# Performance work log

Measured on AMD Instinct MI355X. Metric: run time of the kernel, lower is better.

Reference implementation:

```python
import jax, jax.numpy as jnp
import numpy as np

H = 16  # num heads
ROPE_BASE = 10000.0

def _rope(t):
    # t: [B, T, H, D]; half-split (rotate_half / LLaMA-style) rotary embedding
    B, T, nH, D = t.shape
    half = D // 2
    inv_freq = 1.0 / (ROPE_BASE ** (jnp.arange(0, half, dtype=jnp.float32) / half))
    ang = jnp.arange(T, dtype=jnp.float32)[:, None] * inv_freq[None, :]  # [T, half]
    cos = jnp.cos(ang)[None, :, None, :]  # [1,T,1,half]
    sin = jnp.sin(ang)[None, :, None, :]
    t1, t2 = t[..., :half], t[..., half:]
    return jnp.concatenate([t1 * cos - t2 * sin, t2 * cos + t1 * sin], axis=-1)

def setup_inputs() -> dict:
    key = jax.random.key(0)
    ks = jax.random.split(key, 5)
    B, T, C = 2, 2048, 1024
    s = 1.0 / np.sqrt(C)
    return {
        "x": jax.random.normal(ks[0], (B, T, C), jnp.float32),
        "Wqkv": jax.random.normal(ks[1], (C, 3 * C), jnp.float32) * s,
        "bqkv": jnp.zeros((3 * C,), jnp.float32),
        "Wout": jax.random.normal(ks[2], (C, C), jnp.float32) * s,
        "bout": jnp.zeros((C,), jnp.float32),
    }

def reference(x, Wqkv, bqkv, Wout, bout):
    B, T, C = x.shape
    D = C // H
    qkv = (x @ Wqkv + bqkv).reshape(B, T, 3, H, D)
    q, k, v = qkv[:, :, 0], qkv[:, :, 1], qkv[:, :, 2]  # [B,T,H,D]
    q = _rope(q)
    k = _rope(k)
    scale = 1.0 / jnp.sqrt(jnp.asarray(D, x.dtype))
    scores = jnp.einsum('bqhd,bkhd->bhqk', q, k) * scale
    probs = jax.nn.softmax(scores, axis=-1)
    attn = jnp.einsum('bhqk,bkhd->bqhd', probs, v).reshape(B, T, C)
    return attn @ Wout + bout
```

## Files before the change

### kernel.cpp

```cpp
#include <hip/hip_runtime.h>

typedef float f32x4 __attribute__((ext_vector_type(4)));
typedef short bf16x8 __attribute__((ext_vector_type(8)));
typedef short bf16x4 __attribute__((ext_vector_type(4)));

#define DEV __device__ __forceinline__

DEV unsigned short f2bf(float x) {
  union { float f; unsigned u; } v; v.f = x;
  unsigned r = v.u + 0x7fffu + ((v.u >> 16) & 1u);
  return (unsigned short)(r >> 16);
}
DEV float bf2f(unsigned short h) {
  union { unsigned u; float f; } v; v.u = ((unsigned)h) << 16;
  return v.f;
}

#if defined(__has_builtin)
# if __has_builtin(__builtin_amdgcn_global_load_lds)
#  define HAVE_GLL 1
# endif
# if __has_builtin(__builtin_amdgcn_exp2f)
#  define EXP2(x) __builtin_amdgcn_exp2f(x)
# else
#  define EXP2(x) exp2f(x)
# endif
#else
# define EXP2(x) exp2f(x)
#endif

DEV unsigned pk_bf16_trunc(float a, float b) {
  return __builtin_amdgcn_perm(__float_as_uint(b), __float_as_uint(a), 0x07060302u);
}
DEV unsigned pk_bf16_rnd(float a, float b) {
  return ((unsigned)f2bf(b) << 16) | f2bf(a);
}

DEV void g2l16(const unsigned short* g, unsigned short* l) {
#ifdef HAVE_GLL
  __builtin_amdgcn_global_load_lds((const __attribute__((address_space(1))) void*)g,
                                   (__attribute__((address_space(3))) void*)l, 16, 0, 0);
#else
  *(uint4*)l = *(const uint4*)g;
#endif
}

DEV f32x4 mfma16x16x16(bf16x4 a, bf16x4 b, f32x4 c) {
#if defined(__has_builtin) && __has_builtin(__builtin_amdgcn_mfma_f32_16x16x16bf16_1k)
  return __builtin_amdgcn_mfma_f32_16x16x16bf16_1k(a, b, c, 0, 0, 0);
#else
  asm volatile("v_mfma_f32_16x16x16_bf16 %0, %1, %2, %0" : "+v"(c) : "v"(a), "v"(b));
  return c;
#endif
}

__global__ void rope_tab(float* cosb, float* sinb) {
  int i = blockIdx.x * 256 + threadIdx.x;
  int t = i >> 5, d = i & 31;
  float invf = (float)(1.0 / pow(10000.0, (double)d / 32.0));
  float ang = (float)t * invf;
  cosb[i] = (float)cos((double)ang);
  sinb[i] = (float)sin((double)ang);
}

__global__ void castA(const float* __restrict__ in, unsigned short* __restrict__ out) {
  int i = blockIdx.x * 256 + threadIdx.x;
  f32x4 v = ((const f32x4*)in)[i];
  ushort4 o;
  o.x = f2bf(v[0]); o.y = f2bf(v[1]); o.z = f2bf(v[2]); o.w = f2bf(v[3]);
  ((ushort4*)out)[i] = o;
}

__global__ __launch_bounds__(256) void transW(const float* __restrict__ W,
                                              unsigned short* __restrict__ Wt, int N) {
  __shared__ float t[64 * 65];
  int k0 = blockIdx.x * 64, n0 = blockIdx.y * 64;
  for (int idx = threadIdx.x; idx < 4096; idx += 256) {
    int kl = idx >> 6, nl = idx & 63;
    t[kl * 65 + nl] = W[(size_t)(k0 + kl) * N + n0 + nl];
  }
  __syncthreads();
  for (int idx = threadIdx.x; idx < 4096; idx += 256) {
    int nl = idx >> 6, kl = idx & 63;
    Wt[(size_t)(n0 + nl) * 1024 + k0 + kl] = f2bf(t[kl * 65 + nl]);
  }
}

#define QSCALE 0.180336880f
__global__ __launch_bounds__(256, 2) void gemm_qkv(
    const unsigned short* __restrict__ A, const unsigned short* __restrict__ Bt,
    const float* __restrict__ bias, const float* __restrict__ cosb,
    const float* __restrict__ sinb, unsigned short* __restrict__ QK,
    unsigned short* __restrict__ Vt) {
  const int K = 1024;
  __shared__ alignas(16) unsigned short As[128 * 64];
  __shared__ alignas(16) unsigned short Bs[128 * 64];
  const int tid = threadIdx.x;
  const int lane = tid & 63, wave = tid >> 6;
  const int l15 = lane & 15, quad = lane >> 4;
  const int m0 = blockIdx.y * 128, n0 = blockIdx.x * 128;
  const int wm = (wave & 1) * 64, wn = (wave >> 1) * 64;

  f32x4 acc[4][4];
#pragma unroll
  for (int i = 0; i < 4; i++)
#pragma unroll
    for (int j = 0; j < 4; j++)
#pragma unroll
      for (int r = 0; r < 4; r++) acc[i][j][r] = 0.f;

  for (int kt = 0; kt < 16; ++kt) {
    __syncthreads();
#pragma unroll
    for (int i = 0; i < 4; ++i) {
      int u = i * 256 + tid;
      int row = u >> 3;
      int kcg = (u & 7) ^ (row & 7);
      g2l16(A  + (size_t)(m0 + row) * K + (kt << 6) + (kcg << 3), As + u * 8);
      g2l16(Bt + (size_t)(n0 + row) * K + (kt << 6) + (kcg << 3), Bs + u * 8);
    }
    __syncthreads();
#pragma unroll
    for (int ks = 0; ks < 2; ++ks) {
      const int kc = ks * 4 + quad;
      bf16x8 af[4], bfr[4];
#pragma unroll
      for (int t = 0; t < 4; ++t) {
        int mrow = wm + t * 16 + l15;
        af[t] = *(const bf16x8*)(As + (mrow * 8 + (kc ^ (mrow & 7))) * 8);
        int nrow = wn + t * 16 + l15;
        bfr[t] = *(const bf16x8*)(Bs + (nrow * 8 + (kc ^ (nrow & 7))) * 8);
      }
#pragma unroll
      for (int mt = 0; mt < 4; ++mt)
#pragma unroll
        for (int nt = 0; nt < 4; ++nt)
          acc[mt][nt] = __builtin_amdgcn_mfma_f32_16x16x32_bf16(af[mt], bfr[nt], acc[mt][nt], 0, 0, 0);
    }
  }
  const int headcol = n0 + wn;
  const int b = m0 >> 11;
  float bb[4];
#pragma unroll
  for (int nt = 0; nt < 4; ++nt) bb[nt] = bias[headcol + nt * 16 + l15];

  if (headcol < 2048) {
    const float scale = (headcol < 1024) ? QSCALE : 1.f;
#pragma unroll
    for (int mt = 0; mt < 4; ++mt) {
#pragma unroll
      for (int r = 0; r < 4; ++r) {
        int row = m0 + wm + mt * 16 + quad * 4 + r;
        int t = row & 2047;
#pragma unroll
        for (int nt = 0; nt < 2; ++nt) {
          int d = nt * 16 + l15;
          float c = cosb[t * 32 + d], s = sinb[t * 32 + d];
          float v1 = acc[mt][nt][r] + bb[nt];
          float v2 = acc[mt][nt + 2][r] + bb[nt + 2];
          QK[(size_t)row * 2048 + headcol + d]      = f2bf((v1 * c - v2 * s) * scale);
          QK[(size_t)row * 2048 + headcol + d + 32] = f2bf((v2 * c + v1 * s) * scale);
        }
      }
    }
  } else {
    const int hv = (headcol - 2048) >> 6;
    const int t0 = (m0 + wm) & 2047;
#pragma unroll
    for (int mt = 0; mt < 4; ++mt)
#pragma unroll
      for (int nt = 0; nt < 4; ++nt) {
        int d = nt * 16 + l15;
        uint2 w;
        w.x = pk_bf16_rnd(acc[mt][nt][0] + bb[nt], acc[mt][nt][1] + bb[nt]);
        w.y = pk_bf16_rnd(acc[mt][nt][2] + bb[nt], acc[mt][nt][3] + bb[nt]);
        *(uint2*)(Vt + ((size_t)((b * 16 + hv) * 64 + d)) * 2048 + t0 + mt * 16 + quad * 4) = w;
      }
  }
}

__global__ __launch_bounds__(256, 2) void gemm64(
    const unsigned short* __restrict__ A, const unsigned short* __restrict__ Bt,
    const float* __restrict__ bias, float* __restrict__ C, int M, int N, int K) {
  __shared__ alignas(16) unsigned short As[64 * 64];
  __shared__ alignas(16) unsigned short Bs[128 * 64];
  const int tid = threadIdx.x;
  const int lane = tid & 63, wave = tid >> 6;
  const int l15 = lane & 15, quad = lane >> 4;
  const int m0 = blockIdx.y * 64, n0 = blockIdx.x * 128;
  const int wm = (wave & 1) * 32, wn = (wave >> 1) * 64;

  f32x4 acc[2][4];
#pragma unroll
  for (int i = 0; i < 2; i++)
#pragma unroll
    for (int j = 0; j < 4; j++)
#pragma unroll
      for (int r = 0; r < 4; r++) acc[i][j][r] = 0.f;

  const int nkt = K >> 6;
  for (int kt = 0; kt < nkt; ++kt) {
    __syncthreads();
#pragma unroll
    for (int i = 0; i < 2; ++i) {
      int u = i * 256 + tid;
      int row = u >> 3;
      int kcg = (u & 7) ^ (row & 7);
      g2l16(A + (size_t)(m0 + row) * K + (kt << 6) + (kcg << 3), As + u * 8);
    }
#pragma unroll
    for (int i = 0; i < 4; ++i) {
      int u = i * 256 + tid;
      int row = u >> 3;
      int kcg = (u & 7) ^ (row & 7);
      g2l16(Bt + (size_t)(n0 + row) * K + (kt << 6) + (kcg << 3), Bs + u * 8);
    }
    __syncthreads();
#pragma unroll
    for (int ks = 0; ks < 2; ++ks) {
      const int kc = ks * 4 + quad;
      bf16x8 af[2], bfr[4];
#pragma unroll
      for (int t = 0; t < 2; ++t) {
        int mrow = wm + t * 16 + l15;
        af[t] = *(const bf16x8*)(As + (mrow * 8 + (kc ^ (mrow & 7))) * 8);
      }
#pragma unroll
      for (int t = 0; t < 4; ++t) {
        int nrow = wn + t * 16 + l15;
        bfr[t] = *(const bf16x8*)(Bs + (nrow * 8 + (kc ^ (nrow & 7))) * 8);
      }
#pragma unroll
      for (int mt = 0; mt < 2; ++mt)
#pragma unroll
        for (int nt = 0; nt < 4; ++nt)
          acc[mt][nt] = __builtin_amdgcn_mfma_f32_16x16x32_bf16(af[mt], bfr[nt], acc[mt][nt], 0, 0, 0);
    }
  }
#pragma unroll
  for (int mt = 0; mt < 2; ++mt)
#pragma unroll
    for (int nt = 0; nt < 4; ++nt) {
      int col = n0 + wn + nt * 16 + l15;
      int rowb = m0 + wm + mt * 16 + quad * 4;
      float b = bias[col];
#pragma unroll
      for (int r = 0; r < 4; ++r)
        C[(size_t)(rowb + r) * N + col] = acc[mt][nt][r] + b;
    }
}

__global__ __launch_bounds__(128, 2) void flash_attn(const unsigned short* __restrict__ QK,
                                                     const unsigned short* __restrict__ Vt,
                                                     unsigned short* __restrict__ O) {
  __shared__ alignas(16) unsigned short Ks[64 * 64];
  __shared__ alignas(16) unsigned short Vs[64 * 64];
  const int tid = threadIdx.x, lane = tid & 63, wave = tid >> 6;
  const int l15 = lane & 15, quad = lane >> 4;
  const int bh = blockIdx.x, qb = blockIdx.y;
  const int b = bh >> 4, h = bh & 15;
  const int q0 = qb * 64 + wave * 32;
  bf16x8 qf[2][2];
#pragma unroll
  for (int ks = 0; ks < 2; ++ks)
#pragma unroll
    for (int qg = 0; qg < 2; ++qg)
      qf[ks][qg] = *(const bf16x8*)(QK + (size_t)(b * 2048 + q0 + qg * 16 + l15) * 2048 +
                                    h * 64 + ks * 32 + quad * 8);
  f32x4 o[2][4];
#pragma unroll
  for (int qg = 0; qg < 2; qg++)
#pragma unroll
    for (int nt = 0; nt < 4; nt++)
#pragma unroll
      for (int r = 0; r < 4; r++) o[qg][nt][r] = 0.f;
  float li[2] = {0.f, 0.f};
  const f32x4 negb = {-12.f, -12.f, -12.f, -12.f};

  for (int kb = 0; kb < 32; ++kb) {
    __syncthreads();
#pragma unroll
    for (int i = 0; i < 4; ++i) {
      int u = i * 128 + tid;
      int row = u >> 3;
      int cg = (u & 7) ^ (row & 7);
      g2l16(QK + (size_t)(b * 2048 + kb * 64 + row) * 2048 + 1024 + h * 64 + cg * 8, Ks + u * 8);
      g2l16(Vt + ((size_t)bh * 64 + row) * 2048 + kb * 64 + cg * 8, Vs + u * 8);
    }
    __syncthreads();
    f32x4 sacc[2][4];
#pragma unroll
    for (int ks = 0; ks < 2; ++ks) {
      const int kc = ks * 4 + quad;
#pragma unroll
      for (int mt = 0; mt < 4; ++mt) {
        int key = mt * 16 + l15;
        bf16x8 kf = *(const bf16x8*)(Ks + (key * 8 + (kc ^ (key & 7))) * 8);
        if (ks == 0) {
          sacc[0][mt] = __builtin_amdgcn_mfma_f32_16x16x32_bf16(kf, qf[0][0], negb, 0, 0, 0);
          sacc[1][mt] = __builtin_amdgcn_mfma_f32_16x16x32_bf16(kf, qf[0][1], negb, 0, 0, 0);
        } else {
          sacc[0][mt] = __builtin_amdgcn_mfma_f32_16x16x32_bf16(kf, qf[1][0], sacc[0][mt], 0, 0, 0);
          sacc[1][mt] = __builtin_amdgcn_mfma_f32_16x16x32_bf16(kf, qf[1][1], sacc[1][mt], 0, 0, 0);
        }
      }
    }
    bf16x4 vf[4][4];
#pragma unroll
    for (int nt = 0; nt < 4; ++nt)
#pragma unroll
      for (int mt = 0; mt < 4; ++mt) {
        int dd = nt * 16 + l15;
        int cg = mt * 2 + (quad >> 1);
        vf[nt][mt] = *(const bf16x4*)(Vs + (dd * 8 + (cg ^ (dd & 7))) * 8 + (quad & 1) * 4);
      }
#pragma unroll
    for (int qg = 0; qg < 2; ++qg) {
      bf16x4 pf[4];
      float psum = 0.f;
#pragma unroll
      for (int mt = 0; mt < 4; ++mt) {
        float p0 = EXP2(sacc[qg][mt][0]);
        float p1 = EXP2(sacc[qg][mt][1]);
        float p2 = EXP2(sacc[qg][mt][2]);
        float p3 = EXP2(sacc[qg][mt][3]);
        psum += (p0 + p1) + (p2 + p3);
        union { uint2 u; bf16x4 v; } cc;
        cc.u.x = pk_bf16_trunc(p0, p1);
        cc.u.y = pk_bf16_trunc(p2, p3);
        pf[mt] = cc.v;
      }
      li[qg] += psum;
#pragma unroll
      for (int nt = 0; nt < 4; ++nt)
#pragma unroll
        for (int mt = 0; mt < 4; ++mt)
          o[qg][nt] = mfma16x16x16(vf[nt][mt], pf[mt], o[qg][nt]);
    }
  }
#pragma unroll
  for (int qg = 0; qg < 2; ++qg) {
    li[qg] += __shfl_xor(li[qg], 16);
    li[qg] += __shfl_xor(li[qg], 32);
    float inv = 1.001953125f / li[qg];
    size_t rowb = (size_t)(b * 2048 + q0 + qg * 16 + l15) * 1024 + h * 64;
#pragma unroll
    for (int nt = 0; nt < 4; ++nt) {
      uint2 w;
      w.x = pk_bf16_rnd(o[qg][nt][0] * inv, o[qg][nt][1] * inv);
      w.y = pk_bf16_rnd(o[qg][nt][2] * inv, o[qg][nt][3] * inv);
      *(uint2*)(O + rowb + nt * 16 + quad * 4) = w;
    }
  }
}

extern "C" void kernel_launch(void* const* d_in, const int* in_sizes, int n_in,
                              void* d_out, int out_size, void* d_ws, size_t ws_size,
                              hipStream_t stream) {
  const float* x    = (const float*)d_in[0];
  const float* Wqkv = (const float*)d_in[1];
  const float* bqkv = (const float*)d_in[2];
  const float* Wout = (const float*)d_in[3];
  const float* bout = (const float*)d_in[4];
  float* out = (float*)d_out;
  char* ws = (char*)d_ws;
  float*          COS  = (float*)(ws + 0);
  float*          SIN  = (float*)(ws + 262144);
  unsigned short* A1   = (unsigned short*)(ws + 524288);
  unsigned short* W1t  = (unsigned short*)(ws + 8912896);
  unsigned short* W2t  = (unsigned short*)(ws + 15204352);
  unsigned short* QK   = (unsigned short*)(ws + 17301504);
  unsigned short* VT   = (unsigned short*)(ws + 34078720);
  unsigned short* A2   = (unsigned short*)(ws + 42467328);

  rope_tab<<<256, 256, 0, stream>>>(COS, SIN);
  castA<<<4096, 256, 0, stream>>>(x, A1);
  transW<<<dim3(16, 48), 256, 0, stream>>>(Wqkv, W1t, 3072);
  transW<<<dim3(16, 16), 256, 0, stream>>>(Wout, W2t, 1024);
  gemm_qkv<<<dim3(24, 32), 256, 0, stream>>>(A1, W1t, bqkv, COS, SIN, QK, VT);
  flash_attn<<<dim3(32, 32), 128, 0, stream>>>(QK, VT, A2);
  gemm64<<<dim3(8, 64), 256, 0, stream>>>(A2, W2t, bout, out, 4096, 1024, 1024);
}
```

Measured before the change: 191.5 us.

## Fuse prep kernels into one launch and enlarge flash-attention tiles to 128x128

After: 181.5 us. 5.2% less time.

```diff
diff --git a/kernel.cpp b/kernel.cpp
--- a/kernel.cpp
+++ b/kernel.cpp
@@ -54,27 +54,36 @@
 #endif
 }
 
-__global__ void rope_tab(float* cosb, float* sinb) {
-  int i = blockIdx.x * 256 + threadIdx.x;
-  int t = i >> 5, d = i & 31;
-  float invf = (float)(1.0 / pow(10000.0, (double)d / 32.0));
-  float ang = (float)t * invf;
-  cosb[i] = (float)cos((double)ang);
-  sinb[i] = (float)sin((double)ang);
-}
-
-__global__ void castA(const float* __restrict__ in, unsigned short* __restrict__ out) {
-  int i = blockIdx.x * 256 + threadIdx.x;
-  f32x4 v = ((const f32x4*)in)[i];
-  ushort4 o;
-  o.x = f2bf(v[0]); o.y = f2bf(v[1]); o.z = f2bf(v[2]); o.w = f2bf(v[3]);
-  ((ushort4*)out)[i] = o;
-}
-
-__global__ __launch_bounds__(256) void transW(const float* __restrict__ W,
-                                              unsigned short* __restrict__ Wt, int N) {
+__global__ __launch_bounds__(256) void prep(const float* __restrict__ x,
+                                            const float* __restrict__ Wqkv,
+                                            const float* __restrict__ Wout,
+                                            float* cosb, float* sinb,
+                                            unsigned short* __restrict__ A1,
+                                            unsigned short* __restrict__ W1t,
+                                            unsigned short* __restrict__ W2t) {
   __shared__ float t[64 * 65];
-  int k0 = blockIdx.x * 64, n0 = blockIdx.y * 64;
+  int blk = blockIdx.x;
+  if (blk < 256) {
+    int i = blk * 256 + threadIdx.x;
+    int tt = i >> 5, d = i & 31;
+    float invf = (float)(1.0 / pow(10000.0, (double)d / 32.0));
+    float ang = (float)tt * invf;
+    cosb[i] = (float)cos((double)ang);
+    sinb[i] = (float)sin((double)ang);
+    return;
+  }
+  if (blk < 4352) {
+    int i = (blk - 256) * 256 + threadIdx.x;
+    f32x4 v = ((const f32x4*)x)[i];
+    ushort4 o;
+    o.x = f2bf(v[0]); o.y = f2bf(v[1]); o.z = f2bf(v[2]); o.w = f2bf(v[3]);
+    ((ushort4*)A1)[i] = o;
+    return;
+  }
+  const float* W; unsigned short* Wt; int N, bidx;
+  if (blk < 5120) { W = Wqkv; Wt = W1t; N = 3072; bidx = blk - 4352; }
+  else            { W = Wout; Wt = W2t; N = 1024; bidx = blk - 5120; }
+  int k0 = (bidx & 15) * 64, n0 = (bidx >> 4) * 64;
   for (int idx = threadIdx.x; idx < 4096; idx += 256) {
     int kl = idx >> 6, nl = idx & 63;
     t[kl * 65 + nl] = W[(size_t)(k0 + kl) * N + n0 + nl];
@@ -250,16 +259,16 @@
     }
 }
 
-__global__ __launch_bounds__(128, 2) void flash_attn(const unsigned short* __restrict__ QK,
+__global__ __launch_bounds__(256, 2) void flash_attn(const unsigned short* __restrict__ QK,
                                                      const unsigned short* __restrict__ Vt,
                                                      unsigned short* __restrict__ O) {
-  __shared__ alignas(16) unsigned short Ks[64 * 64];
-  __shared__ alignas(16) unsigned short Vs[64 * 64];
+  __shared__ alignas(16) unsigned short Ks[128 * 64];
+  __shared__ alignas(16) unsigned short Vs[64 * 128];
   const int tid = threadIdx.x, lane = tid & 63, wave = tid >> 6;
   const int l15 = lane & 15, quad = lane >> 4;
   const int bh = blockIdx.x, qb = blockIdx.y;
   const int b = bh >> 4, h = bh & 15;
-  const int q0 = qb * 64 + wave * 32;
+  const int q0 = qb * 128 + wave * 32;
   bf16x8 qf[2][2];
 #pragma unroll
   for (int ks = 0; ks < 2; ++ks)
@@ -277,23 +286,26 @@
   float li[2] = {0.f, 0.f};
   const f32x4 negb = {-12.f, -12.f, -12.f, -12.f};
 
-  for (int kb = 0; kb < 32; ++kb) {
+  for (int kb = 0; kb < 16; ++kb) {
     __syncthreads();
 #pragma unroll
     for (int i = 0; i < 4; ++i) {
-      int u = i * 128 + tid;
-      int row = u >> 3;
-      int cg = (u & 7) ^ (row & 7);
-      g2l16(QK + (size_t)(b * 2048 + kb * 64 + row) * 2048 + 1024 + h * 64 + cg * 8, Ks + u * 8);
-      g2l16(Vt + ((size_t)bh * 64 + row) * 2048 + kb * 64 + cg * 8, Vs + u * 8);
-    }
-    __syncthreads();
-    f32x4 sacc[2][4];
+      int u = i * 256 + tid;
+      int krow = u >> 3;
+      int kcg = (u & 7) ^ (krow & 7);
+      g2l16(QK + (size_t)(b * 2048 + kb * 128 + krow) * 2048 + 1024 + h * 64 + kcg * 8,
+            Ks + u * 8);
+      int vrow = u >> 4;
+      int vcg = (u & 15) ^ (vrow & 7);
+      g2l16(Vt + ((size_t)bh * 64 + vrow) * 2048 + kb * 128 + vcg * 8, Vs + u * 8);
+    }
+    __syncthreads();
+    f32x4 sacc[2][8];
 #pragma unroll
     for (int ks = 0; ks < 2; ++ks) {
       const int kc = ks * 4 + quad;
 #pragma unroll
-      for (int mt = 0; mt < 4; ++mt) {
+      for (int mt = 0; mt < 8; ++mt) {
         int key = mt * 16 + l15;
         bf16x8 kf = *(const bf16x8*)(Ks + (key * 8 + (kc ^ (key & 7))) * 8);
         if (ks == 0) {
@@ -305,21 +317,12 @@
         }
       }
     }
-    bf16x4 vf[4][4];
-#pragma unroll
-    for (int nt = 0; nt < 4; ++nt)
-#pragma unroll
-      for (int mt = 0; mt < 4; ++mt) {
-        int dd = nt * 16 + l15;
-        int cg = mt * 2 + (quad >> 1);
-        vf[nt][mt] = *(const bf16x4*)(Vs + (dd * 8 + (cg ^ (dd & 7))) * 8 + (quad & 1) * 4);
-      }
+    bf16x4 pf[2][8];
 #pragma unroll
     for (int qg = 0; qg < 2; ++qg) {
-      bf16x4 pf[4];
       float psum = 0.f;
 #pragma unroll
-      for (int mt = 0; mt < 4; ++mt) {
+      for (int mt = 0; mt < 8; ++mt) {
         float p0 = EXP2(sacc[qg][mt][0]);
         float p1 = EXP2(sacc[qg][mt][1]);
         float p2 = EXP2(sacc[qg][mt][2]);
@@ -328,14 +331,20 @@
         union { uint2 u; bf16x4 v; } cc;
         cc.u.x = pk_bf16_trunc(p0, p1);
         cc.u.y = pk_bf16_trunc(p2, p3);
-        pf[mt] = cc.v;
+        pf[qg][mt] = cc.v;
       }
       li[qg] += psum;
-#pragma unroll
-      for (int nt = 0; nt < 4; ++nt)
-#pragma unroll
-        for (int mt = 0; mt < 4; ++mt)
-          o[qg][nt] = mfma16x16x16(vf[nt][mt], pf[mt], o[qg][nt]);
+    }
+#pragma unroll
+    for (int mt = 0; mt < 8; ++mt) {
+      const int cu = mt * 2 + (quad >> 1);
+#pragma unroll
+      for (int nt = 0; nt < 4; ++nt) {
+        int dd = nt * 16 + l15;
+        bf16x4 vf = *(const bf16x4*)(Vs + (dd * 16 + (cu ^ (dd & 7))) * 8 + (quad & 1) * 4);
+        o[0][nt] = mfma16x16x16(vf, pf[0][mt], o[0][nt]);
+        o[1][nt] = mfma16x16x16(vf, pf[1][mt], o[1][nt]);
+      }
     }
   }
 #pragma unroll
@@ -373,11 +382,8 @@
   unsigned short* VT   = (unsigned short*)(ws + 34078720);
   unsigned short* A2   = (unsigned short*)(ws + 42467328);
 
-  rope_tab<<<256, 256, 0, stream>>>(COS, SIN);
-  castA<<<4096, 256, 0, stream>>>(x, A1);
-  transW<<<dim3(16, 48), 256, 0, stream>>>(Wqkv, W1t, 3072);
-  transW<<<dim3(16, 16), 256, 0, stream>>>(Wout, W2t, 1024);
+  prep<<<5376, 256, 0, stream>>>(x, Wqkv, Wout, COS, SIN, A1, W1t, W2t);
   gemm_qkv<<<dim3(24, 32), 256, 0, stream>>>(A1, W1t, bqkv, COS, SIN, QK, VT);
-  flash_attn<<<dim3(32, 32), 128, 0, stream>>>(QK, VT, A2);
+  flash_attn<<<dim3(32, 16), 256, 0, stream>>>(QK, VT, A2);
   gemm64<<<dim3(8, 64), 256, 0, stream>>>(A2, W2t, bout, out, 4096, 1024, 1024);
 }
```
